# Performance work log

Hardware: AMD Instinct MI355X
Metric: run time of the kernel (lower is better)

The kernel has to match this reference:

```python
import jax, jax.numpy as jnp
import numpy as np

DIM_GATE = 256
DIM_BIAS = 128
H = 8
D = 32
EPS = 1e-5


def _layernorm(t, gamma, beta):
    mu = jnp.mean(t, axis=-1, keepdims=True)
    var = jnp.mean(jnp.square(t - mu), axis=-1, keepdims=True)
    return (t - mu) * jax.lax.rsqrt(var + EPS) * gamma + beta


def setup_inputs() -> dict:
    key = jax.random.key(0)
    ks = jax.random.split(key, 12)
    b, l = 2, 512
    x = jax.random.normal(ks[0], (b, l, DIM_GATE), dtype=jnp.float32)
    bias = jax.random.normal(ks[1], (b, l, l, DIM_BIAS), dtype=jnp.float32)
    s_g = 1.0 / np.sqrt(DIM_GATE)
    s_b = 1.0 / np.sqrt(DIM_BIAS)
    return {
        "x": x,
        "bias": bias,
        "g_gamma": jnp.ones((DIM_GATE,), jnp.float32),
        "g_beta": jnp.zeros((DIM_GATE,), jnp.float32),
        "b_gamma": jnp.ones((DIM_BIAS,), jnp.float32),
        "b_beta": jnp.zeros((DIM_BIAS,), jnp.float32),
        "Wq": jax.random.normal(ks[2], (DIM_GATE, H * D), jnp.float32) * s_g,
        "Wk": jax.random.normal(ks[3], (DIM_GATE, H * D), jnp.float32) * s_g,
        "Wv": jax.random.normal(ks[4], (DIM_GATE, H * D), jnp.float32) * s_g,
        "Wb": jax.random.normal(ks[5], (DIM_BIAS, H), jnp.float32) * s_b,
        "Wg": jax.random.normal(ks[6], (DIM_GATE, H * D), jnp.float32) * s_g,
        "bg": jnp.zeros((H * D,), jnp.float32),
        "Wout": jax.random.normal(ks[7], (H * D, DIM_GATE), jnp.float32) * s_g,
        "bout": jnp.zeros((DIM_GATE,), jnp.float32),
    }


def reference(x, bias, g_gamma, g_beta, b_gamma, b_beta, Wq, Wk, Wv, Wb, Wg, bg, Wout, bout):
    b, l, _ = x.shape
    scaling = 1.0 / np.sqrt(D)
    xn = _layernorm(x, g_gamma, g_beta)                      # [b,l,dg]
    bn = _layernorm(bias, b_gamma, b_beta)                   # [b,l,l,db]
    q = (xn @ Wq).reshape(b, l, H, D)                        # [b,l,h,d]
    k = (xn @ Wk).reshape(b, l, H, D) * scaling
    v = (xn @ Wv).reshape(b, l, H, D)
    pair_b = bn @ Wb                                         # [b,q,k,h]
    gate = jax.nn.sigmoid(xn @ Wg + bg)                      # [b,l,h*d]
    attn = jnp.einsum('bqhd,bkhd->bqkh', q, k) + pair_b      # [b,q,k,h]
    attn = jax.nn.softmax(attn, axis=-2)                     # softmax over k
    out = jnp.einsum('bqkh,bkhd->bqhd', attn, v).reshape(b, l, H * D)
    out = gate * out
    return out @ Wout + bout
```

## Files before the change

kernel.cpp:

```cpp
#include <hip/hip_runtime.h>
#include <math.h>

#define LSEQ 512
#define DG 256
#define DB 128
#define NH 8
#define HD 32
#define EPSV 1e-5f
#define LP2 516

typedef __attribute__((ext_vector_type(8))) short bf16x8;
typedef __attribute__((ext_vector_type(4))) float f32x4;

__device__ __forceinline__ unsigned short f2bf(float x) {
    unsigned int u = __float_as_uint(x);
    u += 0x7FFFu + ((u >> 16) & 1u);
    return (unsigned short)(u >> 16);
}
__device__ __forceinline__ float bf2f(unsigned short h) {
    return __uint_as_float(((unsigned int)h) << 16);
}

__global__ __launch_bounds__(256) void prep_kernel(
    const float* __restrict__ x, const float* __restrict__ g_gamma,
    const float* __restrict__ g_beta, const float* __restrict__ Wq,
    const float* __restrict__ Wk, const float* __restrict__ Wv,
    const float* __restrict__ Wg, const float* __restrict__ bg,
    float* __restrict__ q_ws, float* __restrict__ k_ws,
    float* __restrict__ v_ws, float* __restrict__ g_ws)
{
    __shared__ float xs[4][DG];
    const int t = threadIdx.x;
    const int wave = t >> 6, lane = t & 63;
    const int row0 = blockIdx.x << 2;

    {
        const int row = row0 + wave;
        const float4 xv = *(const float4*)(x + (size_t)row * DG + lane * 4);
        float s  = xv.x + xv.y + xv.z + xv.w;
        float ss = xv.x*xv.x + xv.y*xv.y + xv.z*xv.z + xv.w*xv.w;
        #pragma unroll
        for (int m = 32; m >= 1; m >>= 1) { s += __shfl_xor(s, m); ss += __shfl_xor(ss, m); }
        const float mean = s * (1.f / DG);
        const float rstd = rsqrtf(ss * (1.f / DG) - mean * mean + EPSV);
        const float4 gg = *(const float4*)(g_gamma + lane * 4);
        const float4 gb = *(const float4*)(g_beta + lane * 4);
        float4 xo;
        xo.x = (xv.x - mean) * rstd * gg.x + gb.x;
        xo.y = (xv.y - mean) * rstd * gg.y + gb.y;
        xo.z = (xv.z - mean) * rstd * gg.z + gb.z;
        xo.w = (xv.w - mean) * rstd * gg.w + gb.w;
        *(float4*)&xs[wave][lane * 4] = xo;
    }
    __syncthreads();

    float aq[4] = {0,0,0,0}, ak[4] = {0,0,0,0}, av[4] = {0,0,0,0}, ag[4] = {0,0,0,0};
    #pragma unroll 4
    for (int c = 0; c < DG; ++c) {
        const float wq = Wq[(size_t)c * DG + t];
        const float wk = Wk[(size_t)c * DG + t];
        const float wv = Wv[(size_t)c * DG + t];
        const float wg = Wg[(size_t)c * DG + t];
        #pragma unroll
        for (int r = 0; r < 4; ++r) {
            const float xr = xs[r][c];
            aq[r] = fmaf(xr, wq, aq[r]);
            ak[r] = fmaf(xr, wk, ak[r]);
            av[r] = fmaf(xr, wv, av[r]);
            ag[r] = fmaf(xr, wg, ag[r]);
        }
    }

    const float scal = 0.17677669529663687f;
    const float bgv = bg[t];
    #pragma unroll
    for (int r = 0; r < 4; ++r) {
        const size_t o = (size_t)(row0 + r) * DG + t;
        q_ws[o] = aq[r];
        k_ws[o] = ak[r] * scal;
        v_ws[o] = av[r];
        g_ws[o] = 1.f / (1.f + __expf(-(ag[r] + bgv)));
    }
}

__global__ __launch_bounds__(256, 3) void fused_kernel(
    const float* __restrict__ bias, const float* __restrict__ b_gamma,
    const float* __restrict__ b_beta, const float* __restrict__ Wb,
    const float* __restrict__ Wout, const float* __restrict__ bout,
    const float* __restrict__ q_ws, const float* __restrict__ k_ws,
    const float* __restrict__ v_ws, const float* __restrict__ g_ws,
    float* __restrict__ out)
{
    __shared__ float stg[4 * 2048];
    __shared__ float lg[NH * LP2];
    float* ps    = stg;
    float* row_s = stg + 1024;
    float* rden  = stg + 1280;

    const int t = threadIdx.x;
    const int w = t >> 6, l = t & 63;
    const int n = l & 15, quad = l >> 4;
    const int bq = blockIdx.x;
    const int b = bq >> 9;

    bf16x8 gwhi[4], gwlo[4];
    float S1 = 0.f, S0 = 0.f;
    #pragma unroll
    for (int ks = 0; ks < 4; ++ks) {
        #pragma unroll
        for (int j = 0; j < 8; ++j) {
            const int c = ks * 32 + quad * 8 + j;
            const float wb = (n < 8) ? Wb[c * 8 + n] : 0.f;
            const float wv = b_gamma[c] * wb;
            S1 += wv;
            S0 += b_beta[c] * wb;
            unsigned short hi = f2bf(wv);
            unsigned short lo = f2bf(wv - bf2f(hi));
            if (n == 8) { hi = 0x3F80; lo = 0; }
            gwhi[ks][j] = (short)hi;
            gwlo[ks][j] = (short)lo;
        }
    }
    S1 += __shfl_xor(S1, 16); S1 += __shfl_xor(S1, 32);
    S0 += __shfl_xor(S0, 16); S0 += __shfl_xor(S0, 32);

    float* myl = stg + w * 2048;
    const size_t rowbase = (size_t)bq * LSEQ + w * 16;

    auto stage = [&](int tt) {
        const float* src = bias + (rowbase + (size_t)tt * 64) * DB;
        #pragma unroll
        for (int i = 0; i < 8; ++i) {
            __builtin_amdgcn_global_load_lds(
                (const __attribute__((address_space(1))) void*)(src + i * 256 + l * 4),
                (__attribute__((address_space(3))) void*)(myl + i * 256 + l * 4),
                16, 0, 0);
        }
    };

    auto compute = [&](int tt) {
        const float* d = myl + n * 128 + quad * 8;
        f32x4 acc = {0.f, 0.f, 0.f, 0.f};
        float ssq = 0.f;
        #pragma unroll
        for (int ks = 0; ks < 4; ++ks) {
            const float4 x0 = *(const float4*)(d + ks * 32);
            const float4 x1 = *(const float4*)(d + ks * 32 + 4);
            ssq = fmaf(x0.x,x0.x, fmaf(x0.y,x0.y, fmaf(x0.z,x0.z, fmaf(x0.w,x0.w, ssq))));
            ssq = fmaf(x1.x,x1.x, fmaf(x1.y,x1.y, fmaf(x1.z,x1.z, fmaf(x1.w,x1.w, ssq))));
            const float xsv[8] = {x0.x,x0.y,x0.z,x0.w,x1.x,x1.y,x1.z,x1.w};
            bf16x8 ahi, alo;
            #pragma unroll
            for (int j = 0; j < 8; ++j) {
                const unsigned short hi = f2bf(xsv[j]);
                ahi[j] = (short)hi;
                alo[j] = (short)f2bf(xsv[j] - bf2f(hi));
            }
            acc = __builtin_amdgcn_mfma_f32_16x16x32_bf16(ahi, gwhi[ks], acc, 0, 0, 0);
            acc = __builtin_amdgcn_mfma_f32_16x16x32_bf16(alo, gwhi[ks], acc, 0, 0, 0);
            acc = __builtin_amdgcn_mfma_f32_16x16x32_bf16(ahi, gwlo[ks], acc, 0, 0, 0);
        }
        ssq += __shfl_xor(ssq, 16);
        ssq += __shfl_xor(ssq, 32);
        float* pl = lg + n * LP2 + (w * 16 + tt * 64 + quad * 4);
        #pragma unroll
        for (int reg = 0; reg < 4; ++reg) {
            const float sumr = __uint_as_float((unsigned)__builtin_amdgcn_ds_bpermute(
                (quad * 16 + 8) * 4, (int)__float_as_uint(acc[reg])));
            const float ssqr = __uint_as_float((unsigned)__builtin_amdgcn_ds_bpermute(
                (quad * 4 + reg) * 4, (int)__float_as_uint(ssq)));
            const float mean = sumr * (1.f / DB);
            const float var  = ssqr * (1.f / DB) - mean * mean;
            const float rstd = rsqrtf(var + EPSV);
            const float p = rstd * (acc[reg] - mean * S1) + S0;
            if (n < NH) pl[reg] += p;
        }
    };

    stage(0);

    {
        const int d4 = l >> 3, r = l & 7;
        #pragma unroll
        for (int p = 0; p < 2; ++p) {
            const int h = w * 2 + p;
            const float4 qa = *(const float4*)(q_ws + (size_t)bq * DG + h * HD + d4 * 4);
            const float* kbase = k_ws + ((size_t)(b * LSEQ)) * DG + h * HD + d4 * 4;
            float* lrow = lg + h * LP2;
            #pragma unroll 8
            for (int kb8 = 0; kb8 < 64; ++kb8) {
                const int krow = kb8 * 8 + r;
                const float4 kv = *(const float4*)(kbase + (size_t)krow * DG);
                float a0 = fmaf(kv.x, qa.x, fmaf(kv.y, qa.y, fmaf(kv.z, qa.z, kv.w * qa.w)));
                a0 += __shfl_xor(a0, 8);
                a0 += __shfl_xor(a0, 16);
                a0 += __shfl_xor(a0, 32);
                if (d4 == 0) lrow[krow] = a0;
            }
        }
    }
    __syncthreads();

    #pragma unroll
    for (int tt = 0; tt < 8; ++tt) {
        asm volatile("s_waitcnt vmcnt(0)" ::: "memory");
        compute(tt);
        if (tt < 7) {
            asm volatile("s_waitcnt lgkmcnt(0)" ::: "memory");
            stage(tt + 1);
        }
    }
    __syncthreads();

    {
        const int qh = t >> 5, l32 = t & 31;
        float* lrow = lg + qh * LP2;
        float mx = -1e30f;
        #pragma unroll
        for (int i = 0; i < 16; ++i) mx = fmaxf(mx, lrow[l32 + i * 32]);
        #pragma unroll
        for (int m = 16; m >= 1; m >>= 1) mx = fmaxf(mx, __shfl_xor(mx, m));
        float s = 0.f;
        #pragma unroll
        for (int i = 0; i < 16; ++i) {
            const int k = l32 + i * 32;
            const float e = __expf(lrow[k] - mx);
            lrow[k] = e;
            s += e;
        }
        #pragma unroll
        for (int m = 16; m >= 1; m >>= 1) s += __shfl_xor(s, m);
        if (l32 == 0) rden[qh] = 1.f / s;
    }
    __syncthreads();

    {
        const int s4 = t >> 6, c4 = t & 63;
        const int h = c4 >> 3;
        const float* vb = v_ws + ((size_t)(b * LSEQ + s4 * 128)) * DG + c4 * 4;
        const float* prow = lg + h * LP2 + s4 * 128;
        float4 a = {0.f, 0.f, 0.f, 0.f};
        #pragma unroll 8
        for (int i = 0; i < 128; ++i) {
            const float p = prow[i];
            const float4 vv = *(const float4*)(vb + (size_t)i * DG);
            a.x = fmaf(p, vv.x, a.x);
            a.y = fmaf(p, vv.y, a.y);
            a.z = fmaf(p, vv.z, a.z);
            a.w = fmaf(p, vv.w, a.w);
        }
        *(float4*)&ps[(s4 * 64 + c4) * 4] = a;
    }
    __syncthreads();
    if (t < 64) {
        const int c4 = t, h = c4 >> 3;
        float4 a = *(const float4*)&ps[(0 * 64 + c4) * 4];
        #pragma unroll
        for (int s4 = 1; s4 < 4; ++s4) {
            const float4 p4 = *(const float4*)&ps[(s4 * 64 + c4) * 4];
            a.x += p4.x; a.y += p4.y; a.z += p4.z; a.w += p4.w;
        }
        const float sc = rden[h];
        const float4 g4 = *(const float4*)(g_ws + (size_t)bq * DG + c4 * 4);
        float* rs = row_s + c4 * 4;
        rs[0] = a.x * sc * g4.x;
        rs[1] = a.y * sc * g4.y;
        rs[2] = a.z * sc * g4.z;
        rs[3] = a.w * sc * g4.w;
    }
    __syncthreads();

    {
        const int co = t;
        const float* wo = Wout + co;
        float a = 0.f;
        #pragma unroll 8
        for (int c = 0; c < DG; ++c)
            a = fmaf(row_s[c], wo[(size_t)c * DG], a);
        out[(size_t)bq * DG + co] = a + bout[co];
    }
}

extern "C" void kernel_launch(void* const* d_in, const int* in_sizes, int n_in,
                              void* d_out, int out_size, void* d_ws, size_t ws_size,
                              hipStream_t stream)
{
    const float* x       = (const float*)d_in[0];
    const float* bias    = (const float*)d_in[1];
    const float* g_gamma = (const float*)d_in[2];
    const float* g_beta  = (const float*)d_in[3];
    const float* b_gamma = (const float*)d_in[4];
    const float* b_beta  = (const float*)d_in[5];
    const float* Wq      = (const float*)d_in[6];
    const float* Wk      = (const float*)d_in[7];
    const float* Wv      = (const float*)d_in[8];
    const float* Wb      = (const float*)d_in[9];
    const float* Wg      = (const float*)d_in[10];
    const float* bg      = (const float*)d_in[11];
    const float* Wout    = (const float*)d_in[12];
    const float* bout    = (const float*)d_in[13];
    float* out = (float*)d_out;

    float* ws   = (float*)d_ws;
    float* q_ws = ws;
    float* k_ws = ws + 262144;
    float* v_ws = ws + 2 * 262144;
    float* g_ws = ws + 3 * 262144;

    hipLaunchKernelGGL(prep_kernel, dim3(256), dim3(256), 0, stream,
                       x, g_gamma, g_beta, Wq, Wk, Wv, Wg, bg,
                       q_ws, k_ws, v_ws, g_ws);
    hipLaunchKernelGGL(fused_kernel, dim3(1024), dim3(256), 0, stream,
                       bias, b_gamma, b_beta, Wb, Wout, bout,
                       q_ws, k_ws, v_ws, g_ws, out);
}
```

Before: 548.4 us.

## Register-prefetch bias tiles with swizzled LDS stores and split-K output projection

Replaces the direct global-to-LDS async loads of bias tiles with register double-buffering: the next tile is loaded into registers while the current one is written to LDS using an XOR swizzle that the compute reads match, which avoids LDS bank conflicts. The output projection now splits the 256-long reduction across the four waves, with each lane handling four output columns via float4 Wout loads, and combines the partial sums through shared memory. The change trades extra VGPR pressure from the 16 float4 buffers, which may reduce occupancy under launch_bounds(256,3), for better overlap and fewer conflicts.

After: 628.9 us. +14.7%, slower.

```diff
diff --git a/kernel.cpp b/kernel.cpp
--- a/kernel.cpp
+++ b/kernel.cpp
@@ -96,6 +96,7 @@
     float* ps    = stg;
     float* row_s = stg + 1024;
     float* rden  = stg + 1280;
+    float* wps   = stg + 1536;
 
     const int t = threadIdx.x;
     const int w = t >> 6, l = t & 63;
@@ -127,25 +128,21 @@
     float* myl = stg + w * 2048;
     const size_t rowbase = (size_t)bq * LSEQ + w * 16;
 
-    auto stage = [&](int tt) {
-        const float* src = bias + (rowbase + (size_t)tt * 64) * DB;
-        #pragma unroll
-        for (int i = 0; i < 8; ++i) {
-            __builtin_amdgcn_global_load_lds(
-                (const __attribute__((address_space(1))) void*)(src + i * 256 + l * 4),
-                (__attribute__((address_space(3))) void*)(myl + i * 256 + l * 4),
-                16, 0, 0);
-        }
+    auto loadt = [&](float4 (&r)[8], int tt) {
+        const float* src = bias + (rowbase + (size_t)tt * 64) * DB + l * 4;
+        #pragma unroll
+        for (int i = 0; i < 8; ++i) r[i] = *(const float4*)(src + i * 256);
     };
 
     auto compute = [&](int tt) {
-        const float* d = myl + n * 128 + quad * 8;
+        const int xm = ((n & 3) << 3) | (n & 4);
+        const float* dbase = myl + n * 128;
         f32x4 acc = {0.f, 0.f, 0.f, 0.f};
         float ssq = 0.f;
         #pragma unroll
         for (int ks = 0; ks < 4; ++ks) {
-            const float4 x0 = *(const float4*)(d + ks * 32);
-            const float4 x1 = *(const float4*)(d + ks * 32 + 4);
+            const float4 x0 = *(const float4*)(dbase + ((quad * 8 + ks * 32) ^ xm));
+            const float4 x1 = *(const float4*)(dbase + ((quad * 8 + ks * 32 + 4) ^ xm));
             ssq = fmaf(x0.x,x0.x, fmaf(x0.y,x0.y, fmaf(x0.z,x0.z, fmaf(x0.w,x0.w, ssq))));
             ssq = fmaf(x1.x,x1.x, fmaf(x1.y,x1.y, fmaf(x1.z,x1.z, fmaf(x1.w,x1.w, ssq))));
             const float xsv[8] = {x0.x,x0.y,x0.z,x0.w,x1.x,x1.y,x1.z,x1.w};
@@ -177,7 +174,8 @@
         }
     };
 
-    stage(0);
+    float4 rg[8], nx[8];
+    loadt(rg, 0);
 
     {
         const int d4 = l >> 3, r = l & 7;
@@ -203,11 +201,18 @@
 
     #pragma unroll
     for (int tt = 0; tt < 8; ++tt) {
-        asm volatile("s_waitcnt vmcnt(0)" ::: "memory");
+        if (tt < 7) loadt(nx, tt + 1);
+        #pragma unroll
+        for (int i = 0; i < 8; ++i) {
+            const int af = i * 256 + l * 4;
+            const int row = af >> 7;
+            const int xw = ((row & 3) << 3) | (row & 4);
+            *(float4*)(myl + (af ^ xw)) = rg[i];
+        }
         compute(tt);
         if (tt < 7) {
-            asm volatile("s_waitcnt lgkmcnt(0)" ::: "memory");
-            stage(tt + 1);
+            #pragma unroll
+            for (int j = 0; j < 8; ++j) rg[j] = nx[j];
         }
     }
     __syncthreads();
@@ -271,13 +276,23 @@
     __syncthreads();
 
     {
-        const int co = t;
-        const float* wo = Wout + co;
-        float a = 0.f;
+        const int co4 = l;
+        float4 a = {0.f, 0.f, 0.f, 0.f};
         #pragma unroll 8
-        for (int c = 0; c < DG; ++c)
-            a = fmaf(row_s[c], wo[(size_t)c * DG], a);
-        out[(size_t)bq * DG + co] = a + bout[co];
+        for (int c = 0; c < 64; ++c) {
+            const float rs = row_s[w * 64 + c];
+            const float4 wv = *(const float4*)(Wout + (size_t)(w * 64 + c) * DG + co4 * 4);
+            a.x = fmaf(rs, wv.x, a.x);
+            a.y = fmaf(rs, wv.y, a.y);
+            a.z = fmaf(rs, wv.z, a.z);
+            a.w = fmaf(rs, wv.w, a.w);
+        }
+        *(float4*)&wps[w * 256 + co4 * 4] = a;
+    }
+    __syncthreads();
+    {
+        const float a = wps[t] + wps[256 + t] + wps[512 + t] + wps[768 + t];
+        out[(size_t)bq * DG + t] = a + bout[t];
     }
 }
 
```
